# Optimization experiments

Measured on AMD Instinct MI355X. Metric: run time of the kernel, lower is better.

Reference implementation:

```python
import jax, jax.numpy as jnp
import numpy as np

B, S, V, D, H, F, GH, NC, L = 64, 256, 50000, 1024, 16, 4096, 100, 7, 4
DH = D // H


def _ln(x, g, b):
    m = x.mean(-1, keepdims=True)
    v = x.var(-1, keepdims=True)
    return (x - m) / jnp.sqrt(v + 1e-5) * g + b


def setup_inputs() -> dict:
    key = jax.random.key(0)
    ks = iter(jax.random.split(key, 40))
    nrm = lambda shp, s=0.02: jax.random.normal(next(ks), shp, jnp.float32) * s
    inp = {}
    inp["src"] = jax.random.randint(next(ks), (B, S), 0, V)
    inp["em_seq"] = jax.random.normal(next(ks), (B, S, 7), jnp.float32)
    inp["d_ids"] = jax.random.randint(next(ks), (B, 1), 0, B)
    inp["ut_len"] = jax.random.randint(next(ks), (B,), 1, S + 1)
    inp["emb"] = jax.random.uniform(next(ks), (V, D), jnp.float32, -0.1, 0.1)
    inp["Wqkv"] = nrm((L, 3 * D, D)); inp["bqkv"] = jnp.zeros((L, 3 * D), jnp.float32)
    inp["Wo"] = nrm((L, D, D)); inp["bo"] = jnp.zeros((L, D), jnp.float32)
    inp["W1"] = nrm((L, F, D)); inp["b1"] = jnp.zeros((L, F), jnp.float32)
    inp["W2"] = nrm((L, D, F)); inp["b2"] = jnp.zeros((L, D), jnp.float32)
    inp["ln1_g"] = jnp.ones((L, D), jnp.float32); inp["ln1_b"] = jnp.zeros((L, D), jnp.float32)
    inp["ln2_g"] = jnp.ones((L, D), jnp.float32); inp["ln2_b"] = jnp.zeros((L, D), jnp.float32)
    inp["gru_Wih"] = nrm((3 * GH, 7), 0.1); inp["gru_Whh"] = nrm((3 * GH, GH), 0.1)
    inp["gru_bih"] = jnp.zeros((3 * GH,), jnp.float32); inp["gru_bhh"] = jnp.zeros((3 * GH,), jnp.float32)
    inp["dec_W"] = jax.random.uniform(next(ks), (NC, 2 * D + GH), jnp.float32, -0.1, 0.1)
    inp["dec_b"] = jnp.zeros((NC,), jnp.float32)
    return inp


def reference(src, em_seq, d_ids, ut_len, emb, Wqkv, bqkv, Wo, bo, W1, b1, W2, b2,
              ln1_g, ln1_b, ln2_g, ln2_b, gru_Wih, gru_Whh, gru_bih, gru_bhh,
              dec_W, dec_b):
    # embedding + scale + sinusoidal positional encoding
    x = emb[src] * jnp.sqrt(jnp.float32(D))                      # [B,S,D]
    pos = jnp.arange(S, dtype=jnp.float32)[:, None]
    div = jnp.exp(jnp.arange(0, D, 2, dtype=jnp.float32) * (-jnp.log(10000.0) / D))
    pe = jnp.stack([jnp.sin(pos * div), jnp.cos(pos * div)], -1).reshape(S, D)
    x = x + pe

    causal = jnp.tril(jnp.ones((S, S), bool))
    neg = jnp.finfo(x.dtype).min
    for l in range(L):  # post-norm transformer encoder layers (PyTorch default)
        qkv = x @ Wqkv[l].T + bqkv[l]
        q, k, v = jnp.split(qkv, 3, -1)
        q = q.reshape(B, S, H, DH); k = k.reshape(B, S, H, DH); v = v.reshape(B, S, H, DH)
        sc = jnp.einsum('bqhd,bkhd->bhqk', q, k) / jnp.sqrt(jnp.float32(DH))
        sc = jnp.where(causal, sc, neg)
        a = jax.nn.softmax(sc, -1)
        o = jnp.einsum('bhqk,bkhd->bqhd', a, v).reshape(B, S, D)
        x = _ln(x + o @ Wo[l].T + bo[l], ln1_g[l], ln1_b[l])
        ff = jax.nn.relu(x @ W1[l].T + b1[l]) @ W2[l].T + b2[l]
        x = _ln(x + ff, ln2_g[l], ln2_b[l])

    # emotion GRU (PyTorch GRU equations), scan over time
    xp = jnp.einsum('bsf,gf->sbg', em_seq, gru_Wih) + gru_bih    # [S,B,3*GH]

    def step(h, xt):
        hp = h @ gru_Whh.T + gru_bhh
        xr, xz, xn = jnp.split(xt, 3, -1)
        hr, hz, hn = jnp.split(hp, 3, -1)
        r = jax.nn.sigmoid(xr + hr)
        z = jax.nn.sigmoid(xz + hz)
        n = jnp.tanh(xn + r * hn)
        h = (1.0 - z) * n + z * h
        return h, h

    _, hs = jax.lax.scan(step, jnp.zeros((B, GH), x.dtype), xp)
    emo = hs.transpose(1, 0, 2)                                  # [B,S,GH]

    # ragged gather of the 'main' utterance per dialogue + broadcast-concat
    lens = ut_len[d_ids[:, 0]]                                   # [B]
    main = x[jnp.arange(B), lens - 1]                            # [B,D]
    pair = jnp.concatenate([x, jnp.broadcast_to(main[:, None, :], (B, S, D))], -1)
    valid = (jnp.arange(S)[None, :] < lens[:, None])[..., None]
    pair = jnp.where(valid, pair, 0.0)                           # zeros beyond ut_len, as in torch loop
    dec_ip = jnp.concatenate([pair, emo], -1)                    # [B,S,2D+GH]
    return dec_ip @ dec_W.T + dec_b                              # [B,S,NC]
```

## Files before the change

kernel.cpp:

```cpp
#include <hip/hip_runtime.h>
#include <hip/hip_bf16.h>
#include <math.h>

#define BB 64
#define SS 256
#define DD 1024
#define HH 16
#define FFN 4096
#define GHH 100
#define NCC 7
#define LL 4
#define TT (BB*SS)
#define DHH 64

typedef unsigned short u16;
typedef unsigned int u32;
typedef __attribute__((ext_vector_type(4))) float f32x4;
typedef __attribute__((ext_vector_type(8))) short s16x8;
typedef __attribute__((ext_vector_type(4))) unsigned short u16x4;

__device__ __forceinline__ u16 f2bf(float f) {
  union { float f; u32 u; } x; x.f = f;
  u32 r = x.u + 0x7FFFu + ((x.u >> 16) & 1u);
  return (u16)(r >> 16);
}
__device__ __forceinline__ float bf2f(u16 b) {
  union { u32 u; float f; } x; x.u = ((u32)b) << 16;
  return x.f;
}
__device__ __forceinline__ u32 pkbf(float a, float b) {
  return (u32)f2bf(a) | ((u32)f2bf(b) << 16);
}
__device__ __forceinline__ float lo16(u32 u) {
  union { u32 u; float f; } x; x.u = u << 16; return x.f;
}
__device__ __forceinline__ float hi16(u32 u) {
  union { u32 u; float f; } x; x.u = u & 0xffff0000u; return x.f;
}

__global__ void k_f2bf4(const float* __restrict__ s0, u16* __restrict__ d0, int n0,
                        const float* __restrict__ s1, u16* __restrict__ d1, int n1,
                        const float* __restrict__ s2, u16* __restrict__ d2, int n2,
                        const float* __restrict__ s3, u16* __restrict__ d3, int n3) {
  int stride = gridDim.x * blockDim.x;
  int total = n0 + n1 + n2 + n3;
  for (int i = blockIdx.x * blockDim.x + threadIdx.x; i < total; i += stride) {
    const float* s; u16* d; int j = i;
    if (j < n0) { s = s0; d = d0; }
    else {
      j -= n0;
      if (j < n1) { s = s1; d = d1; }
      else {
        j -= n1;
        if (j < n2) { s = s2; d = d2; }
        else { j -= n2; s = s3; d = d3; }
      }
    }
    f32x4 v = *(const f32x4*)(s + (size_t)j * 4);
    u16x4 o;
    o[0] = f2bf(v[0]); o[1] = f2bf(v[1]); o[2] = f2bf(v[2]); o[3] = f2bf(v[3]);
    *(u16x4*)(d + (size_t)j * 4) = o;
  }
}

__global__ void k_pe(float* __restrict__ pe) {
  int i = blockIdx.x * blockDim.x + threadIdx.x;
  if (i >= SS * DD / 2) return;
  int s = i / (DD / 2), j = i % (DD / 2);
  float div = __expf((float)(2 * j) * (-9.210340371976184f / (float)DD));
  float a = (float)s * div;
  pe[s * DD + 2 * j]     = sinf(a);
  pe[s * DD + 2 * j + 1] = cosf(a);
}

__global__ void k_embed(const int* __restrict__ src, const float* __restrict__ emb,
                        const float* __restrict__ pe, u16* __restrict__ xb) {
  int i = blockIdx.x * blockDim.x + threadIdx.x;
  if (i >= TT * DD / 4) return;
  int t = i / (DD / 4);
  int d4 = (i % (DD / 4)) * 4;
  int s = t % SS;
  int tok = src[t];
  f32x4 e = *(const f32x4*)(emb + (size_t)tok * DD + d4);
  f32x4 p = *(const f32x4*)(pe + (size_t)s * DD + d4);
  u16x4 o;
  o[0] = f2bf(e[0] * 32.0f + p[0]); o[1] = f2bf(e[1] * 32.0f + p[1]);
  o[2] = f2bf(e[2] * 32.0f + p[2]); o[3] = f2bf(e[3] * 32.0f + p[3]);
  *(u16x4*)(xb + (size_t)t * DD + d4) = o;
}

#define MEMF asm volatile("" ::: "memory")
#define GBAR do { MEMF; __builtin_amdgcn_sched_barrier(0); __builtin_amdgcn_s_barrier(); __builtin_amdgcn_sched_barrier(0); MEMF; } while(0)
#define VMW4 asm volatile("s_waitcnt vmcnt(4)" ::: "memory")

#define STG(P, isB, h, l, buf, kt) \
  __builtin_amdgcn_global_load_lds( \
    (const __attribute__((address_space(1))) u32*)(P[h][l] + (kt)), \
    (__attribute__((address_space(3))) u32*)(smem + (buf)*65536 + (isB)*32768 + (h)*16384 + (l)*8192 + wid*1024), \
    16, 0, 0)

#define LDB(buf) do { \
  _Pragma("unroll") for (int nf = 0; nf < 4; nf++) \
  _Pragma("unroll") for (int kk = 0; kk < 2; kk++) { \
    int rel = (wn*64 + nf*16 + lm)*128 + kk*64 + lg*16; \
    bq[nf][kk] = *(const s16x8*)(smem + (buf)*65536 + 32768 + (rel ^ (((rel>>9)&1)<<5))); \
  } } while(0)

#define LDA(buf, q) do { \
  _Pragma("unroll") for (int ml = 0; ml < 2; ml++) \
  _Pragma("unroll") for (int kk = 0; kk < 2; kk++) { \
    int rel = (wm*128 + ((q)*2+ml)*16 + lm)*128 + kk*64 + lg*16; \
    aq[ml][kk] = *(const s16x8*)(smem + (buf)*65536 + (rel ^ (((rel>>9)&1)<<5))); \
  } } while(0)

#define MFMAQ(q) do { \
  __builtin_amdgcn_s_setprio(1); \
  _Pragma("unroll") for (int ml = 0; ml < 2; ml++) \
  _Pragma("unroll") for (int nf = 0; nf < 4; nf++) \
  _Pragma("unroll") for (int kk = 0; kk < 2; kk++) \
    acc[(q)*2+ml][nf] = __builtin_amdgcn_mfma_f32_16x16x32_bf16(aq[ml][kk], bq[nf][kk], acc[(q)*2+ml][nf], 0, 0, 0); \
  __builtin_amdgcn_s_setprio(0); \
} while(0)

template<int EPI>
__global__ __launch_bounds__(512, 2)
void k_gemm256(const u16* __restrict__ A, const u16* __restrict__ W,
               const float* __restrict__ bias, u16* __restrict__ C,
               int M, int N, int K) {
  extern __shared__ char smem[];
  const int tid = threadIdx.x;
  const int lane = tid & 63;
  const int wid = tid >> 6;
  const int lm = lane & 15, lg = lane >> 4;
  const int wm = wid >> 2, wn = wid & 3;

  const int NB = N >> 8;
  const int nwg = gridDim.x;
  const int bid = blockIdx.x;
  const int cpx = nwg >> 3;
  const int swzb = (bid & 7) * cpx + (bid >> 3);
  const int m0 = (swzb / NB) << 8;
  const int n0 = (swzb % NB) << 8;

  const u16* pA[2][2];
  const u16* pB[2][2];
#pragma unroll
  for (int h = 0; h < 2; h++)
#pragma unroll
    for (int l = 0; l < 2; l++) {
      int rel = h * 16384 + l * 8192 + tid * 16;
      int sb = rel ^ (((rel >> 9) & 1) << 5);
      int grow = sb >> 7;
      int gcol = (sb & 127) >> 1;
      pA[h][l] = A + (size_t)(m0 + grow) * K + gcol;
      pB[h][l] = W + (size_t)(n0 + grow) * K + gcol;
    }

  f32x4 acc[8][4];
#pragma unroll
  for (int i = 0; i < 8; i++)
#pragma unroll
    for (int j = 0; j < 4; j++) acc[i][j] = (f32x4){0.f, 0.f, 0.f, 0.f};

  s16x8 bq[4][2];
  s16x8 aq[2][2];

  const int NT = K >> 6;

  STG(pB,1,0,0,0,0); STG(pB,1,0,1,0,0); STG(pB,1,1,0,0,0); STG(pB,1,1,1,0,0);
  STG(pA,0,0,0,0,0); STG(pA,0,0,1,0,0); STG(pA,0,1,0,0,0); STG(pA,0,1,1,0,0);
  STG(pB,1,0,0,1,64); STG(pB,1,0,1,1,64); STG(pB,1,1,0,1,64); STG(pB,1,1,1,1,64);
  VMW4;
  GBAR;

  for (int i = 0; i < (NT >> 1); i++) {
    const int t1k = (2*i + 1) * 64;
    int t2 = 2*i + 2; if (t2 >= NT) t2 -= NT;
    int t3 = 2*i + 3; if (t3 >= NT) t3 -= NT;
    const int t2k = t2 * 64, t3k = t3 * 64;

    LDB(0); LDA(0,0);
    STG(pA,0,0,0,1,t1k); STG(pA,0,0,1,1,t1k);
    GBAR; MFMAQ(0); GBAR;
    LDA(0,1);
    STG(pA,0,1,0,1,t1k); STG(pA,0,1,1,1,t1k);
    STG(pB,1,0,0,0,t2k); STG(pB,1,0,1,0,t2k);
    GBAR; MFMAQ(1); GBAR;
    LDA(0,2);
    STG(pB,1,1,0,0,t2k); STG(pB,1,1,1,0,t2k);
    GBAR; MFMAQ(2); GBAR;
    LDA(0,3);
    GBAR; MFMAQ(3); VMW4; GBAR;
    LDB(1); LDA(1,0);
    STG(pA,0,0,0,0,t2k); STG(pA,0,0,1,0,t2k);
    GBAR; MFMAQ(0); GBAR;
    LDA(1,1);
    STG(pA,0,1,0,0,t2k); STG(pA,0,1,1,0,t2k);
    GBAR; MFMAQ(1); GBAR;
    LDA(1,2);
    STG(pB,1,0,0,1,t3k); STG(pB,1,0,1,1,t3k);
    GBAR; MFMAQ(2); GBAR;
    LDA(1,3);
    STG(pB,1,1,0,1,t3k); STG(pB,1,1,1,1,t3k);
    GBAR; MFMAQ(3); VMW4; GBAR;
  }

  float bn[4];
#pragma unroll
  for (int nf = 0; nf < 4; nf++) bn[nf] = bias[n0 + wn*64 + nf*16 + lm];
#pragma unroll
  for (int mf = 0; mf < 8; mf++)
#pragma unroll
    for (int nf = 0; nf < 4; nf++) {
      int col = n0 + wn*64 + nf*16 + lm;
#pragma unroll
      for (int r = 0; r < 4; r++) {
        int row = m0 + wm*128 + mf*16 + lg*4 + r;
        float v = acc[mf][nf][r] + bn[nf];
        if (EPI == 1) v = fmaxf(v, 0.f);
        C[(size_t)row * N + col] = f2bf(v);
      }
    }
}

__global__ __launch_bounds__(256, 2)
void k_attn(const u16* __restrict__ qkv, u16* __restrict__ o) {
  const int h = blockIdx.x;
  const int b = blockIdx.y;
  const int lane = threadIdx.x & 63;
  const int w = threadIdx.x >> 6;
  const int lm = lane & 15, lg = lane >> 4;

  __shared__ u16 Ks[64 * 64];
  __shared__ u16 Vt[64 * 64];
  __shared__ u16 Ps[4][64 * 64];

  const size_t tokbase = (size_t)b * SS;

  s16x8 aq[4][2];
#pragma unroll
  for (int mf = 0; mf < 4; mf++) {
    const u16* qrow = qkv + (tokbase + w * 64 + mf * 16 + lm) * 3072 + h * 64;
#pragma unroll
    for (int kk = 0; kk < 2; kk++)
      aq[mf][kk] = *(const s16x8*)(qrow + kk * 32 + lg * 8);
  }

  f32x4 zero = {0.f, 0.f, 0.f, 0.f};
  f32x4 oacc[4][4];
#pragma unroll
  for (int mf = 0; mf < 4; mf++)
#pragma unroll
    for (int df = 0; df < 4; df++) oacc[mf][df] = zero;
  float m_run[16], l_run[16];
#pragma unroll
  for (int r = 0; r < 16; r++) { m_run[r] = -3e38f; l_run[r] = 0.f; }

  for (int kb = 0; kb < 4; kb++) {
    __syncthreads();
    {
      int krow = threadIdx.x >> 2;
      int seg  = (threadIdx.x & 3) * 16;
      const u16* ksrc = qkv + (tokbase + kb * 64 + krow) * 3072 + 1024 + h * 64 + seg;
      s16x8 v0 = *(const s16x8*)(ksrc);
      s16x8 v1 = *(const s16x8*)(ksrc + 8);
      *(s16x8*)&Ks[krow * 64 + seg] = v0;
      *(s16x8*)&Ks[krow * 64 + seg + 8] = v1;
      const u16* vsrc = qkv + (tokbase + kb * 64 + krow) * 3072 + 2048 + h * 64 + seg;
      s16x8 w0 = *(const s16x8*)(vsrc);
      s16x8 w1 = *(const s16x8*)(vsrc + 8);
#pragma unroll
      for (int e = 0; e < 8; e++) {
        Vt[(seg + e) * 64 + krow]     = (u16)w0[e];
        Vt[(seg + 8 + e) * 64 + krow] = (u16)w1[e];
      }
    }
    __syncthreads();
    if (w < kb) continue;

    s16x8 bk[4][2];
#pragma unroll
    for (int nf = 0; nf < 4; nf++)
#pragma unroll
      for (int kk = 0; kk < 2; kk++)
        bk[nf][kk] = *(const s16x8*)&Ks[(nf * 16 + lm) * 64 + kk * 32 + lg * 8];

    const int colbase = kb * 64;
#pragma unroll
    for (int mf = 0; mf < 4; mf++) {
      f32x4 sfr[4];
#pragma unroll
      for (int nf = 0; nf < 4; nf++) {
        f32x4 acc = zero;
#pragma unroll
        for (int kk = 0; kk < 2; kk++)
          acc = __builtin_amdgcn_mfma_f32_16x16x32_bf16(aq[mf][kk], bk[nf][kk], acc, 0, 0, 0);
        sfr[nf] = acc;
      }
      const int rowbase = w * 64 + mf * 16 + lg * 4;
#pragma unroll
      for (int nf = 0; nf < 4; nf++) {
        int col = colbase + nf * 16 + lm;
#pragma unroll
        for (int r = 0; r < 4; r++) {
          float v = sfr[nf][r] * 0.125f;
          sfr[nf][r] = (col <= rowbase + r) ? v : -1e30f;
        }
      }
#pragma unroll
      for (int r = 0; r < 4; r++) {
        float m = fmaxf(fmaxf(sfr[0][r], sfr[1][r]), fmaxf(sfr[2][r], sfr[3][r]));
#pragma unroll
        for (int off = 1; off < 16; off <<= 1) m = fmaxf(m, __shfl_xor(m, off));
        int idx = mf * 4 + r;
        float mnew = fmaxf(m_run[idx], m);
        float fo = __expf(m_run[idx] - mnew);
        m_run[idx] = mnew;
        float ps = 0.f;
#pragma unroll
        for (int nf = 0; nf < 4; nf++) {
          float p = __expf(sfr[nf][r] - mnew);
          sfr[nf][r] = p;
          ps += p;
        }
#pragma unroll
        for (int off = 1; off < 16; off <<= 1) ps += __shfl_xor(ps, off);
        l_run[idx] = l_run[idx] * fo + ps;
#pragma unroll
        for (int df = 0; df < 4; df++) oacc[mf][df][r] *= fo;
      }
#pragma unroll
      for (int nf = 0; nf < 4; nf++)
#pragma unroll
        for (int r = 0; r < 4; r++)
          Ps[w][(mf * 16 + lg * 4 + r) * 64 + nf * 16 + lm] = f2bf(sfr[nf][r]);
    }
    asm volatile("" ::: "memory");
    s16x8 bv[4][2];
#pragma unroll
    for (int df = 0; df < 4; df++)
#pragma unroll
      for (int kk = 0; kk < 2; kk++)
        bv[df][kk] = *(const s16x8*)&Vt[(df * 16 + lm) * 64 + kk * 32 + lg * 8];
#pragma unroll
    for (int mf = 0; mf < 4; mf++) {
      s16x8 pa[2];
#pragma unroll
      for (int kk = 0; kk < 2; kk++)
        pa[kk] = *(const s16x8*)&Ps[w][(mf * 16 + lm) * 64 + kk * 32 + lg * 8];
#pragma unroll
      for (int df = 0; df < 4; df++)
#pragma unroll
        for (int kk = 0; kk < 2; kk++)
          oacc[mf][df] = __builtin_amdgcn_mfma_f32_16x16x32_bf16(pa[kk], bv[df][kk], oacc[mf][df], 0, 0, 0);
    }
  }

#pragma unroll
  for (int mf = 0; mf < 4; mf++)
#pragma unroll
    for (int df = 0; df < 4; df++)
#pragma unroll
      for (int r = 0; r < 4; r++) {
        int row = w * 64 + mf * 16 + lg * 4 + r;
        float val = oacc[mf][df][r] / l_run[mf * 4 + r];
        o[(tokbase + row) * 1024 + h * 64 + df * 16 + lm] = f2bf(val);
      }
}

__global__ __launch_bounds__(256)
void k_ln(u16* __restrict__ xb, const u16* __restrict__ tmp,
          const float* __restrict__ gam, const float* __restrict__ bet) {
  int t = blockIdx.x;
  int tid = threadIdx.x;
  u16x4 a4 = *(const u16x4*)(xb + (size_t)t * DD + tid * 4);
  u16x4 u4 = *(const u16x4*)(tmp + (size_t)t * DD + tid * 4);
  f32x4 v;
#pragma unroll
  for (int e = 0; e < 4; e++) v[e] = bf2f(a4[e]) + bf2f(u4[e]);
  float s = v[0] + v[1] + v[2] + v[3];
  float s2 = v[0]*v[0] + v[1]*v[1] + v[2]*v[2] + v[3]*v[3];
#pragma unroll
  for (int off = 32; off >= 1; off >>= 1) {
    s  += __shfl_xor(s, off);
    s2 += __shfl_xor(s2, off);
  }
  __shared__ float red[8];
  int w = tid >> 6;
  if ((tid & 63) == 0) { red[w] = s; red[4 + w] = s2; }
  __syncthreads();
  s  = red[0] + red[1] + red[2] + red[3];
  s2 = red[4] + red[5] + red[6] + red[7];
  float mean = s * (1.f / 1024.f);
  float var = s2 * (1.f / 1024.f) - mean * mean;
  float rstd = rsqrtf(var + 1e-5f);
  f32x4 g4 = *(const f32x4*)(gam + tid * 4);
  f32x4 b4 = *(const f32x4*)(bet + tid * 4);
  u16x4 yo;
#pragma unroll
  for (int e = 0; e < 4; e++)
    yo[e] = f2bf((v[e] - mean) * rstd * g4[e] + b4[e]);
  *(u16x4*)(xb + (size_t)t * DD + tid * 4) = yo;
}

#define F7(X) X(0) X(1) X(2) X(3) X(4) X(5) X(6)
#define C12(X) X(0) X(1) X(2) X(3) X(4) X(5) X(6) X(7) X(8) X(9) X(10) X(11)

__global__ __launch_bounds__(640, 1)
void k_gru(const float* __restrict__ em, const float* __restrict__ Wih,
           const float* __restrict__ bih, const float* __restrict__ Whh,
           const float* __restrict__ bhh, float* __restrict__ emo) {
  const int b = blockIdx.x;
  const int tid = threadIdx.x;
  const int iraw = tid / 6;
  const int sub = tid - iraw * 6;
  const int g = sub >> 1, half = sub & 1;
  const bool act = iraw < 100;
  const int i = act ? iraw : 99;
  const int grow = g * 100 + i;

  __shared__ __align__(16) float h[2][104];
  __shared__ float vals[400];

  const float* rowP = Whh + (size_t)grow * 100 + half * 50;
#define LW(q) u32 wa##q = pkbf(rowP[4*(q)], rowP[4*(q)+1]); \
              u32 wb##q = pkbf(rowP[4*(q)+2], rowP[4*(q)+3]); \
              asm volatile("" : "+v"(wa##q), "+v"(wb##q));
  C12(LW)
#undef LW
  u32 wt = pkbf(rowP[48], rowP[49]);
  asm volatile("" : "+v"(wt));

#define LI(f) float wi##f = Wih[grow * 7 + (f)];
  F7(LI)
#undef LI
  const float bhhv = bhh[grow];
  const float bihv = bih[grow];

  if (tid < 104) { h[0][tid] = 0.f; h[1][tid] = 0.f; }
  __syncthreads();

  const float* eb = em + (size_t)b * SS * 7;
#define DE(f) float e##f = eb[f];
  F7(DE)
#undef DE

  for (int s = 0; s < SS; ++s) {
    const float* hc = h[s & 1];
    float* hb_next = h[(s & 1) ^ 1];
    float xp = bihv;
#define MI(f) xp += wi##f * e##f;
    F7(MI)
#undef MI
    {
      int sp = (s + 1 < SS) ? s + 1 : s;
#define LE(f) e##f = eb[sp * 7 + (f)];
      F7(LE)
#undef LE
    }
    const float* hbp = hc + half * 52;
    float a0 = 0.f, a1 = 0.f, a2 = 0.f, a3 = 0.f;
#define MC(q) { f32x4 hv = *(const f32x4*)(hbp + 4*(q)); \
    a0 += lo16(wa##q) * hv[0]; a1 += hi16(wa##q) * hv[1]; \
    a2 += lo16(wb##q) * hv[2]; a3 += hi16(wb##q) * hv[3]; }
    C12(MC)
#undef MC
    { a0 += lo16(wt) * hbp[48]; a1 += hi16(wt) * hbp[49]; }
    float a = (a0 + a1) + (a2 + a3);
    a += __shfl_xor(a, 1);
    if (act && half == 0) {
      if (g == 2) { vals[200 + i] = xp; vals[300 + i] = a + bhhv; }
      else        { vals[g * 100 + i] = xp + a + bhhv; }
    }
    __syncthreads();
    if (tid < 100) {
      int slot = tid + (tid >= 50 ? 2 : 0);
      float hold = hc[slot];
      float rr = 1.f / (1.f + __expf(-vals[tid]));
      float zz = 1.f / (1.f + __expf(-vals[100 + tid]));
      float nx = vals[200 + tid] + rr * vals[300 + tid];
      float e2 = __expf(-2.f * fabsf(nx));
      float th = (1.f - e2) / (1.f + e2);
      float nn = copysignf(th, nx);
      float hv = (1.f - zz) * nn + zz * hold;
      hb_next[slot] = hv;
      emo[((size_t)b * SS + s) * GHH + tid] = hv;
    }
    __syncthreads();
  }
}

__global__ void k_main(const int* __restrict__ d_ids, const int* __restrict__ ut_len,
                       const u16* __restrict__ x, const float* __restrict__ decW,
                       float* __restrict__ md) {
  int b = blockIdx.x;
  int lane = threadIdx.x;
  int len = ut_len[d_ids[b]];
  const u16* xr = x + ((size_t)b * SS + (len - 1)) * DD;
  float acc[NCC];
#pragma unroll
  for (int c = 0; c < NCC; c++) acc[c] = 0.f;
  for (int d = lane; d < DD; d += 64) {
    float xv = bf2f(xr[d]);
#pragma unroll
    for (int c = 0; c < NCC; c++) acc[c] += xv * decW[(size_t)c * 2148 + 1024 + d];
  }
#pragma unroll
  for (int c = 0; c < NCC; c++) {
#pragma unroll
    for (int off = 32; off >= 1; off >>= 1) acc[c] += __shfl_xor(acc[c], off);
  }
  if (lane == 0) {
#pragma unroll
    for (int c = 0; c < NCC; c++) md[b * NCC + c] = acc[c];
  }
}

__global__ __launch_bounds__(256)
void k_dec(const u16* __restrict__ x, const float* __restrict__ emo,
           const float* __restrict__ md, const float* __restrict__ decW,
           const float* __restrict__ decb, const int* __restrict__ d_ids,
           const int* __restrict__ ut_len, float* __restrict__ out) {
  int grp = threadIdx.x >> 6, lane = threadIdx.x & 63;
  int t = blockIdx.x * 4 + grp;
  int b = t / SS, s = t % SS;
  int len = ut_len[d_ids[b]];
  bool valid = s < len;
  float acc[NCC];
#pragma unroll
  for (int c = 0; c < NCC; c++) acc[c] = 0.f;
  if (valid) {
    const u16* xrow = x + (size_t)t * DD;
    for (int d = lane; d < DD; d += 64) {
      float xv = bf2f(xrow[d]);
#pragma unroll
      for (int c = 0; c < NCC; c++) acc[c] += xv * decW[(size_t)c * 2148 + d];
    }
  }
  {
    const float* er = emo + (size_t)t * GHH;
    for (int d = lane; d < GHH; d += 64) {
      float ev = er[d];
#pragma unroll
      for (int c = 0; c < NCC; c++) acc[c] += ev * decW[(size_t)c * 2148 + 2048 + d];
    }
  }
#pragma unroll
  for (int c = 0; c < NCC; c++) {
#pragma unroll
    for (int off = 32; off >= 1; off >>= 1) acc[c] += __shfl_xor(acc[c], off);
  }
  if (lane == 0) {
#pragma unroll
    for (int c = 0; c < NCC; c++) {
      float v = acc[c] + (valid ? md[b * NCC + c] : 0.f) + decb[c];
      out[(size_t)t * NCC + c] = v;
    }
  }
}

extern "C" void kernel_launch(void* const* d_in, const int* in_sizes, int n_in,
                              void* d_out, int out_size, void* d_ws, size_t ws_size,
                              hipStream_t stream) {
  const int*   src    = (const int*)d_in[0];
  const float* em_seq = (const float*)d_in[1];
  const int*   d_ids  = (const int*)d_in[2];
  const int*   ut_len = (const int*)d_in[3];
  const float* emb    = (const float*)d_in[4];
  const float* Wqkv   = (const float*)d_in[5];
  const float* bqkv   = (const float*)d_in[6];
  const float* Wo     = (const float*)d_in[7];
  const float* bo     = (const float*)d_in[8];
  const float* W1     = (const float*)d_in[9];
  const float* b1     = (const float*)d_in[10];
  const float* W2     = (const float*)d_in[11];
  const float* b2     = (const float*)d_in[12];
  const float* ln1g   = (const float*)d_in[13];
  const float* ln1b   = (const float*)d_in[14];
  const float* ln2g   = (const float*)d_in[15];
  const float* ln2b   = (const float*)d_in[16];
  const float* gWih   = (const float*)d_in[17];
  const float* gWhh   = (const float*)d_in[18];
  const float* gbih   = (const float*)d_in[19];
  const float* gbhh   = (const float*)d_in[20];
  const float* decW   = (const float*)d_in[21];
  const float* decb   = (const float*)d_in[22];
  float* out = (float*)d_out;

  char* wsp = (char*)d_ws;
  auto take = [&](size_t n) { char* p = wsp; wsp += (n + 255) & ~(size_t)255; return p; };

  u16*   wqkvb = (u16*)take((size_t)3072 * 1024 * 2);
  u16*   wob   = (u16*)take((size_t)1024 * 1024 * 2);
  u16*   w1b   = (u16*)take((size_t)4096 * 1024 * 2);
  u16*   w2b   = (u16*)take((size_t)1024 * 4096 * 2);
  float* pe    = (float*)take((size_t)SS * DD * 4);
  u16*   xb    = (u16*)take((size_t)TT * DD * 2);
  u16*   big   = (u16*)take((size_t)TT * FFN * 2);
  u16*   ob    = (u16*)take((size_t)TT * DD * 2);
  u16*   tmp16 = (u16*)take((size_t)TT * DD * 2);
  float* emo   = (float*)take((size_t)BB * SS * GHH * 4);
  float* md    = (float*)take((size_t)BB * NCC * 4);

  (void)hipFuncSetAttribute((const void*)&k_gemm256<0>,
      hipFuncAttributeMaxDynamicSharedMemorySize, 131072);
  (void)hipFuncSetAttribute((const void*)&k_gemm256<1>,
      hipFuncAttributeMaxDynamicSharedMemorySize, 131072);

  k_gru<<<BB, 640, 0, stream>>>(em_seq, gWih, gbih, gWhh, gbhh, emo);

  k_pe<<<(SS * DD / 2 + 255) / 256, 256, 0, stream>>>(pe);
  k_embed<<<TT * DD / 4 / 256, 256, 0, stream>>>(src, emb, pe, xb);

  for (int l = 0; l < LL; ++l) {
    k_f2bf4<<<2048, 256, 0, stream>>>(
        Wqkv + (size_t)l * 3072 * 1024, wqkvb, 3072 * 1024 / 4,
        Wo   + (size_t)l * 1024 * 1024, wob,   1024 * 1024 / 4,
        W1   + (size_t)l * 4096 * 1024, w1b,   4096 * 1024 / 4,
        W2   + (size_t)l * 1024 * 4096, w2b,   1024 * 4096 / 4);

    k_gemm256<0><<<(TT/256) * (3072/256), 512, 131072, stream>>>(
        xb, wqkvb, bqkv + (size_t)l * 3072, big, TT, 3072, 1024);
    k_attn<<<dim3(HH, BB), 256, 0, stream>>>(big, ob);
    k_gemm256<0><<<(TT/256) * (1024/256), 512, 131072, stream>>>(
        ob, wob, bo + (size_t)l * 1024, tmp16, TT, 1024, 1024);
    k_ln<<<TT, 256, 0, stream>>>(xb, tmp16, ln1g + (size_t)l * DD, ln1b + (size_t)l * DD);
    k_gemm256<1><<<(TT/256) * (4096/256), 512, 131072, stream>>>(
        xb, w1b, b1 + (size_t)l * 4096, big, TT, 4096, 1024);
    k_gemm256<0><<<(TT/256) * (1024/256), 512, 131072, stream>>>(
        big, w2b, b2 + (size_t)l * 1024, tmp16, TT, 1024, 4096);
    k_ln<<<TT, 256, 0, stream>>>(xb, tmp16, ln2g + (size_t)l * DD, ln2b + (size_t)l * DD);
  }

  k_main<<<BB, 64, 0, stream>>>(d_ids, ut_len, xb, decW, md);
  k_dec<<<TT / 4, 256, 0, stream>>>(xb, emo, md, decW, decb, d_ids, ut_len, out);
}
```

Measured before the change: 2.346 ms.

## Restructure GRU kernel to one thread per gate row, dropping a barrier per step

```diff
diff --git a/kernel.cpp b/kernel.cpp
--- a/kernel.cpp
+++ b/kernel.cpp
@@ -404,32 +404,37 @@
 }
 
 #define F7(X) X(0) X(1) X(2) X(3) X(4) X(5) X(6)
-#define C12(X) X(0) X(1) X(2) X(3) X(4) X(5) X(6) X(7) X(8) X(9) X(10) X(11)
-
-__global__ __launch_bounds__(640, 1)
+#define L50(X) X(0) X(1) X(2) X(3) X(4) X(5) X(6) X(7) X(8) X(9) \
+  X(10) X(11) X(12) X(13) X(14) X(15) X(16) X(17) X(18) X(19) \
+  X(20) X(21) X(22) X(23) X(24) X(25) X(26) X(27) X(28) X(29) \
+  X(30) X(31) X(32) X(33) X(34) X(35) X(36) X(37) X(38) X(39) \
+  X(40) X(41) X(42) X(43) X(44) X(45) X(46) X(47) X(48) X(49)
+#define Q25(X) X(0,1,0) X(2,3,1) X(4,5,2) X(6,7,3) X(8,9,4) \
+  X(10,11,5) X(12,13,6) X(14,15,7) X(16,17,8) X(18,19,9) \
+  X(20,21,10) X(22,23,11) X(24,25,12) X(26,27,13) X(28,29,14) \
+  X(30,31,15) X(32,33,16) X(34,35,17) X(36,37,18) X(38,39,19) \
+  X(40,41,20) X(42,43,21) X(44,45,22) X(46,47,23) X(48,49,24)
+
+__global__ __launch_bounds__(448, 1)
 void k_gru(const float* __restrict__ em, const float* __restrict__ Wih,
            const float* __restrict__ bih, const float* __restrict__ Whh,
            const float* __restrict__ bhh, float* __restrict__ emo) {
   const int b = blockIdx.x;
   const int tid = threadIdx.x;
-  const int iraw = tid / 6;
-  const int sub = tid - iraw * 6;
-  const int g = sub >> 1, half = sub & 1;
-  const bool act = iraw < 100;
-  const int i = act ? iraw : 99;
-  const int grow = g * 100 + i;
-
-  __shared__ __align__(16) float h[2][104];
-  __shared__ float vals[400];
-
-  const float* rowP = Whh + (size_t)grow * 100 + half * 50;
-#define LW(q) u32 wa##q = pkbf(rowP[4*(q)], rowP[4*(q)+1]); \
-              u32 wb##q = pkbf(rowP[4*(q)+2], rowP[4*(q)+3]); \
-              asm volatile("" : "+v"(wa##q), "+v"(wb##q));
-  C12(LW)
+  const int uraw = tid >> 2;
+  const int g3 = tid & 3;
+  const bool act = (uraw < 100) && (g3 < 3);
+  const int u = (uraw < 100) ? uraw : 99;
+  const int g = (g3 < 3) ? g3 : 0;
+  const int grow = g * 100 + u;
+
+  __shared__ __align__(16) float h[2][100];
+
+  const float* rowP = Whh + (size_t)grow * 100;
+#define LW(k) u32 w##k = pkbf(rowP[2*(k)], rowP[2*(k)+1]); \
+  asm volatile("" : "+v"(w##k));
+  L50(LW)
 #undef LW
-  u32 wt = pkbf(rowP[48], rowP[49]);
-  asm volatile("" : "+v"(wt));
 
 #define LI(f) float wi##f = Wih[grow * 7 + (f)];
   F7(LI)
@@ -437,7 +442,7 @@
   const float bhhv = bhh[grow];
   const float bihv = bih[grow];
 
-  if (tid < 104) { h[0][tid] = 0.f; h[1][tid] = 0.f; }
+  if (tid < 100) { h[0][tid] = 0.f; h[1][tid] = 0.f; }
   __syncthreads();
 
   const float* eb = em + (size_t)b * SS * 7;
@@ -447,7 +452,7 @@
 
   for (int s = 0; s < SS; ++s) {
     const float* hc = h[s & 1];
-    float* hb_next = h[(s & 1) ^ 1];
+    float* hn_buf = h[(s & 1) ^ 1];
     float xp = bihv;
 #define MI(f) xp += wi##f * e##f;
     F7(MI)
@@ -458,33 +463,29 @@
       F7(LE)
 #undef LE
     }
-    const float* hbp = hc + half * 52;
     float a0 = 0.f, a1 = 0.f, a2 = 0.f, a3 = 0.f;
-#define MC(q) { f32x4 hv = *(const f32x4*)(hbp + 4*(q)); \
-    a0 += lo16(wa##q) * hv[0]; a1 += hi16(wa##q) * hv[1]; \
-    a2 += lo16(wb##q) * hv[2]; a3 += hi16(wb##q) * hv[3]; }
-    C12(MC)
+#define MC(ka, kb2, q) { f32x4 hv = *(const f32x4*)(hc + 4*(q)); \
+    a0 += lo16(w##ka) * hv[0]; a1 += hi16(w##ka) * hv[1]; \
+    a2 += lo16(w##kb2) * hv[2]; a3 += hi16(w##kb2) * hv[3]; }
+    Q25(MC)
 #undef MC
-    { a0 += lo16(wt) * hbp[48]; a1 += hi16(wt) * hbp[49]; }
     float a = (a0 + a1) + (a2 + a3);
-    a += __shfl_xor(a, 1);
-    if (act && half == 0) {
-      if (g == 2) { vals[200 + i] = xp; vals[300 + i] = a + bhhv; }
-      else        { vals[g * 100 + i] = xp + a + bhhv; }
-    }
-    __syncthreads();
-    if (tid < 100) {
-      int slot = tid + (tid >= 50 ? 2 : 0);
-      float hold = hc[slot];
-      float rr = 1.f / (1.f + __expf(-vals[tid]));
-      float zz = 1.f / (1.f + __expf(-vals[100 + tid]));
-      float nx = vals[200 + tid] + rr * vals[300 + tid];
+    float comb = xp + a + bhhv;
+    float nh   = a + bhhv;
+    float zsum = __shfl_xor(comb, 1);
+    float nhid = __shfl_xor(nh, 2);
+    float nxin = __shfl_xor(xp, 2);
+    if (act && g3 == 0) {
+      float hold = hc[u];
+      float rr = 1.f / (1.f + __expf(-comb));
+      float zz = 1.f / (1.f + __expf(-zsum));
+      float nx = nxin + rr * nhid;
       float e2 = __expf(-2.f * fabsf(nx));
       float th = (1.f - e2) / (1.f + e2);
       float nn = copysignf(th, nx);
       float hv = (1.f - zz) * nn + zz * hold;
-      hb_next[slot] = hv;
-      emo[((size_t)b * SS + s) * GHH + tid] = hv;
+      hn_buf[u] = hv;
+      emo[((size_t)b * SS + s) * GHH + u] = hv;
     }
     __syncthreads();
   }
@@ -607,7 +608,7 @@
   (void)hipFuncSetAttribute((const void*)&k_gemm256<1>,
       hipFuncAttributeMaxDynamicSharedMemorySize, 131072);
 
-  k_gru<<<BB, 640, 0, stream>>>(em_seq, gWih, gbih, gWhh, gbhh, emo);
+  k_gru<<<BB, 448, 0, stream>>>(em_seq, gWih, gbih, gWhh, gbhh, emo);
 
   k_pe<<<(SS * DD / 2 + 255) / 256, 256, 0, stream>>>(pe);
   k_embed<<<TT * DD / 4 / 256, 256, 0, stream>>>(src, emb, pe, xb);
```

New measurement: 2.376 ms. About the same (+1.3%).
